# Optimization experiments

Hardware: AMD Instinct MI355X
Metric: run time of the kernel (lower is better)

Reference implementation:

```python
import jax, jax.numpy as jnp
import numpy as np

B, N, D, E = 4, 2048, 1024, 4
H = 4 * D  # expert hidden (mult=4)


def setup_inputs() -> dict:
    key = jax.random.key(0)
    ks = jax.random.split(key, 8)
    std = 0.02
    return {
        "x": jax.random.normal(ks[0], (B, N, D), jnp.float32),
        "W_slot": jax.random.normal(ks[1], (E * D, D), jnp.float32) * std,
        "u_slot": jax.random.normal(ks[2], (D,), jnp.float32),
        "sigma_slot": jnp.ones((1,), jnp.float32),
        "W1": jax.random.normal(ks[3], (E, H, D), jnp.float32) * std,
        "b1": jnp.zeros((E, H), jnp.float32),
        "u1": jax.random.normal(ks[4], (E, D), jnp.float32),
        "sig1": jnp.ones((E,), jnp.float32),
        "W2": jax.random.normal(ks[5], (E, D, H), jnp.float32) * std,
        "b2": jnp.zeros((E, D), jnp.float32),
        "u2": jax.random.normal(ks[6], (E, H), jnp.float32),
        "sig2": jnp.ones((E,), jnp.float32),
    }


def _sn_weight(W, u, sigma):
    # One power-iteration step (no_grad in torch -> stop_gradient), then
    # sigma_spec = v^T W u'; weight = W / sigma_spec * learnable sigma.
    v = W @ u
    v = jax.lax.stop_gradient(v / jnp.linalg.norm(v))
    u2 = W.T @ v
    u2 = jax.lax.stop_gradient(u2 / jnp.linalg.norm(u2))
    s = jnp.einsum('c,cd,d->', v, W, u2)
    return W * (sigma / s)


def reference(x, W_slot, u_slot, sigma_slot, W1, b1, u1, sig1, W2, b2, u2, sig2):
    b, n, d = x.shape
    e = W1.shape[0]
    s = n // e  # slots per expert; n divisible by e -> no padding, no mask

    # dynamic slot embeddings from consecutive-segment means
    Wsl = _sn_weight(W_slot, u_slot, sigma_slot[0])          # [e*d, d]
    xm = x.reshape(b, s, e, d).mean(axis=2)                   # [b, s, d]
    slot_embeds = (xm @ Wsl.T).reshape(b, s, e, d)
    slot_embeds = slot_embeds.transpose(0, 2, 1, 3)           # [b, e, s, d]

    logits = jnp.einsum('bnd,besd->bnes', x, slot_embeds)     # [b, n, e, s]
    dispatch = jax.nn.softmax(logits, axis=1)                 # softmax over n
    combine = jax.nn.softmax(logits.reshape(b, n, e * s), axis=-1)

    slots = jnp.einsum('bnd,bnes->ebsd', x, dispatch)         # [e, b, s, d]

    # per-expert FFN with spectral-normed weights (vectorized over experts)
    W1n = jax.vmap(_sn_weight)(W1, u1, sig1)                  # [e, H, d]
    W2n = jax.vmap(_sn_weight)(W2, u2, sig2)                  # [e, d, H]
    h = jax.nn.gelu(jnp.einsum('ebsd,ehd->ebsh', slots, W1n) + b1[:, None, None, :],
                    approximate=False)
    y = jnp.einsum('ebsh,edh->ebsd', h, W2n) + b2[:, None, None, :]

    out = y.transpose(1, 0, 2, 3).reshape(b, e * s, d)        # [b, e*s, d]
    return jnp.einsum('bsd,bns->bnd', out, combine)           # [b, n, d]
```

## Files before the change

### kernel.cpp

```cpp
#include <hip/hip_runtime.h>
#include <hip/hip_bf16.h>
#include <math.h>

constexpr int CB  = 4;
constexpr int CN  = 2048;
constexpr int CD  = 1024;
constexpr int CE  = 4;
constexpr int CS  = 512;
constexpr int CH  = 4096;
constexpr int CES = 2048;

typedef unsigned short u16;
typedef unsigned int   u32;
typedef __bf16 bf16x8 __attribute__((ext_vector_type(8)));
typedef float  f32x4  __attribute__((ext_vector_type(4)));

__device__ __forceinline__ u16 f2bf(float x) {
  u32 u = __float_as_uint(x);
  u = (u + 0x7FFF + ((u >> 16) & 1)) >> 16;
  return (u16)u;
}

__device__ __forceinline__ void gl2lds16(const void* g, void* l) {
  __builtin_amdgcn_global_load_lds(
      (const __attribute__((address_space(1))) void*)g,
      (__attribute__((address_space(3))) void*)l, 16, 0, 0);
}

__device__ __forceinline__ void xcd_swz(int& bx, int& by, int& bz) {
  u32 gx = gridDim.x, gy = gridDim.y;
  u32 w = blockIdx.x + gx * (blockIdx.y + gy * blockIdx.z);
  u32 nwg = gx * gy * gridDim.z;
  u32 q = nwg >> 3;
  u32 wg = (w & 7) * q + (w >> 3);
  bx = wg % gx;
  u32 r = wg / gx;
  by = r % gy;
  bz = r / gy;
}


__global__ __launch_bounds__(256) void gemv_rows_k(const float* __restrict__ W,
    const float* __restrict__ u, float* __restrict__ t1, int M, int K, int ustride) {
  int bi = blockIdx.y;
  int row = blockIdx.x * 4 + (threadIdx.x >> 6);
  int lane = threadIdx.x & 63;
  const float* Wr = W + ((long)bi * M + row) * K;
  const float* ub = u + (long)bi * ustride;
  float s = 0.f;
  for (int k = lane; k < K; k += 64) s += Wr[k] * ub[k];
#pragma unroll
  for (int off = 32; off; off >>= 1) s += __shfl_down(s, off, 64);
  if (lane == 0) t1[bi * M + row] = s;
}

__global__ __launch_bounds__(256) void gemv_cols_k(const float* __restrict__ W,
    const float* __restrict__ t1, float* __restrict__ t2,
    u16* __restrict__ bh, u16* __restrict__ bl, int M, int K) {
  int bi = blockIdx.z;
  int k = blockIdx.x * 256 + threadIdx.x;
  int m0 = blockIdx.y * 256;
  const float* Wb = W + (long)bi * M * K;
  const float* tb = t1 + bi * M;
  u16* bhb = bh + (long)bi * M * K;
  u16* blb = bl ? bl + (long)bi * M * K : nullptr;
  float s = 0.f;
#pragma unroll 4
  for (int m = 0; m < 256; m++) {
    long idx = (long)(m0 + m) * K + k;
    float w = Wb[idx];
    s += w * tb[m0 + m];
    u16 h = f2bf(w);
    bhb[idx] = h;
    if (blb) blb[idx] = f2bf(w - __uint_as_float((u32)h << 16));
  }
  atomicAdd(&t2[bi * K + k], s);
}

__global__ __launch_bounds__(256) void scale_k(const float* __restrict__ t1,
    const float* __restrict__ t2, const float* __restrict__ sig,
    float* __restrict__ out, int M, int K) {
  int bi = blockIdx.x;
  int tid = threadIdx.x;
  __shared__ float red[256];
  float s1 = 0.f;
  for (int i = tid; i < M; i += 256) { float v = t1[bi * M + i]; s1 += v * v; }
  red[tid] = s1; __syncthreads();
  for (int w = 128; w; w >>= 1) { if (tid < w) red[tid] += red[tid + w]; __syncthreads(); }
  float n1 = red[0]; __syncthreads();
  float s2 = 0.f;
  for (int i = tid; i < K; i += 256) { float v = t2[bi * K + i]; s2 += v * v; }
  red[tid] = s2; __syncthreads();
  for (int w = 128; w; w >>= 1) { if (tid < w) red[tid] += red[tid + w]; __syncthreads(); }
  if (tid == 0) out[bi] = sig[bi] * sqrtf(n1 / red[0]);
}

__global__ __launch_bounds__(256) void xsplit_fused_k(const float* __restrict__ x,
    u16* __restrict__ xh, u16* __restrict__ xl,
    u16* __restrict__ xmh, u16* __restrict__ xml) {
  int idx = blockIdx.x * 256 + threadIdx.x;
  int d8 = idx & (CD / 8 - 1);
  int si = (idx >> 7) & (CS - 1);
  int b  = idx >> 16;
  long rbase = ((long)(b * CN + si * 4)) * CD + d8 * 8;
  float vr[4][8];
#pragma unroll
  for (int r = 0; r < 4; r++) {
    float4 a = *(const float4*)(x + rbase + (long)r * CD);
    float4 c = *(const float4*)(x + rbase + (long)r * CD + 4);
    vr[r][0]=a.x; vr[r][1]=a.y; vr[r][2]=a.z; vr[r][3]=a.w;
    vr[r][4]=c.x; vr[r][5]=c.y; vr[r][6]=c.z; vr[r][7]=c.w;
  }
#pragma unroll
  for (int r = 0; r < 4; r++) {
    u16 oh[8], ol[8];
#pragma unroll
    for (int c = 0; c < 8; c++) {
      u16 h = f2bf(vr[r][c]);
      oh[c] = h;
      ol[c] = f2bf(vr[r][c] - __uint_as_float((u32)h << 16));
    }
    *(uint4*)(xh + rbase + (long)r * CD) = *(const uint4*)oh;
    *(uint4*)(xl + rbase + (long)r * CD) = *(const uint4*)ol;
  }
  long mbase = ((long)(b * CS + si)) * CD + d8 * 8;
  u16 oh[8], ol[8];
#pragma unroll
  for (int c = 0; c < 8; c++) {
    float v = 0.25f * (vr[0][c] + vr[1][c] + vr[2][c] + vr[3][c]);
    u16 h = f2bf(v);
    oh[c] = h;
    ol[c] = f2bf(v - __uint_as_float((u32)h << 16));
  }
  *(uint4*)(xmh + mbase) = *(const uint4*)oh;
  *(uint4*)(xml + mbase) = *(const uint4*)ol;
}

__global__ __launch_bounds__(256) void colstat_part_k(const float* __restrict__ lg,
    float* __restrict__ pmax, float* __restrict__ psum) {
  int es = blockIdx.x * 256 + threadIdx.x;
  int sl = blockIdx.y;
  int b  = blockIdx.z;
  const float* p = lg + ((long)(b * CN + sl * 256)) * CES + es;
  float m = -1e30f, s = 0.f;
  for (int i = 0; i < 256; i++) {
    float v = p[(long)i * CES];
    if (v > m) { s *= __expf(m - v); m = v; }
    s += __expf(v - m);
  }
  int o = (b * 8 + sl) * CES + es;
  pmax[o] = m; psum[o] = s;
}

__global__ __launch_bounds__(256) void colstat_comb_k(const float* __restrict__ pmax,
    const float* __restrict__ psum, float* __restrict__ cmax, float* __restrict__ csum) {
  int idx = blockIdx.x * 256 + threadIdx.x;
  int b = idx >> 11;
  int es = idx & (CES - 1);
  float m = -1e30f;
#pragma unroll
  for (int sl = 0; sl < 8; sl++) m = fmaxf(m, pmax[(b * 8 + sl) * CES + es]);
  float s = 0.f;
#pragma unroll
  for (int sl = 0; sl < 8; sl++)
    s += psum[(b * 8 + sl) * CES + es] * __expf(pmax[(b * 8 + sl) * CES + es] - m);
  cmax[idx] = m; csum[idx] = s;
}

__global__ __launch_bounds__(256) void rowcomb_k(const float* __restrict__ lg,
                                                 u16* __restrict__ outB) {
  __shared__ float red[8];
  long row = blockIdx.x;
  const float* p = lg + row * CES + threadIdx.x * 8;
  float4 a = *(const float4*)p;
  float4 b = *(const float4*)(p + 4);
  float v[8] = {a.x, a.y, a.z, a.w, b.x, b.y, b.z, b.w};
  float m = v[0];
#pragma unroll
  for (int c = 1; c < 8; c++) m = fmaxf(m, v[c]);
#pragma unroll
  for (int off = 32; off; off >>= 1) m = fmaxf(m, __shfl_xor(m, off, 64));
  int wv = threadIdx.x >> 6;
  if ((threadIdx.x & 63) == 0) red[wv] = m;
  __syncthreads();
  m = fmaxf(fmaxf(red[0], red[1]), fmaxf(red[2], red[3]));
  float s = 0.f;
#pragma unroll
  for (int c = 0; c < 8; c++) { v[c] = __expf(v[c] - m); s += v[c]; }
#pragma unroll
  for (int off = 32; off; off >>= 1) s += __shfl_xor(s, off, 64);
  if ((threadIdx.x & 63) == 0) red[4 + wv] = s;
  __syncthreads();
  float inv = 1.f / (red[4] + red[5] + red[6] + red[7]);
  u16 o[8];
#pragma unroll
  for (int c = 0; c < 8; c++) o[c] = f2bf(v[c] * inv);
  *(uint4*)(outB + row * CES + threadIdx.x * 8) = *(const uint4*)o;
}

__global__ __launch_bounds__(256) void tr_f2b_k(const float* __restrict__ in,
    u16* __restrict__ out, const float* __restrict__ sub, int R, int C, int expmode) {
  __shared__ u16 t[32][33];
  int z = blockIdx.z;
  long ibase = (long)z * R * C;
  int r0 = blockIdx.y * 32, c0 = blockIdx.x * 32;
  int tx = threadIdx.x & 31, ty = threadIdx.x >> 5;
  float cm = expmode ? sub[(long)z * C + c0 + tx] : 0.f;
  for (int rr = ty; rr < 32; rr += 8) {
    float v = in[ibase + (long)(r0 + rr) * C + c0 + tx];
    if (expmode) v = __expf(v - cm);
    t[tx][rr] = f2bf(v);
  }
  __syncthreads();
  for (int cc = ty; cc < 32; cc += 8)
    out[ibase + (long)(c0 + cc) * R + r0 + tx] = t[cc][tx];
}

struct MEpSESplit {
  u16* hi; u16* lo; const float* scale;
  __device__ void store(int z, int m, int n, float v) const {
    v *= scale[0];
    int b = m >> 9, si = m & 511, ei = n >> 10, di = n & 1023;
    long o = ((long)(b * CES + ei * 512 + si)) * CD + di;
    u16 h = f2bf(v);
    hi[o] = h;
    lo[o] = f2bf(v - __uint_as_float((u32)h << 16));
  }
};
struct MEpLogits {
  float* lg;
  __device__ void store(int b, int m, int n, float v) const {
    lg[((long)(b * CN + m)) * CES + n] = v;
  }
};
struct MEpSlots {
  u16* sb; const float* __restrict__ csum;
  __device__ void store(int b, int m, int n, float v) const {
    float inv = 1.f / csum[b * CES + m];
    int e = m >> 9, si = m & 511;
    sb[((long)(e * 2048 + b * 512 + si)) * CD + n] = f2bf(v * inv);
  }
};
struct MEpGelu {
  u16* h; const float* __restrict__ scales; const float* __restrict__ b1;
  __device__ void store(int e, int m, int n, float v) const {
    float xg = v * scales[1 + e] + b1[e * CH + n];
    float g = 0.5f * xg * (1.f + erff(xg * 0.70710678118654752f));
    h[((long)(e * 2048 + m)) * CH + n] = f2bf(g);
  }
};
struct MEpYT {
  u16* ot; const float* __restrict__ scales; const float* __restrict__ b2;
  __device__ void store(int e, int m, int n, float v) const {
    int b = n >> 9, si = n & 511;
    ot[((long)(b * CD + m)) * CES + e * 512 + si] = f2bf(v * scales[5 + e] + b2[e * CD + m]);
  }
};
struct MEpOut {
  float* o;
  __device__ void store(int b, int m, int n, float v) const {
    o[((long)(b * CN + m)) * CD + n] = v;
  }
};


template <int BN, int BK, class EP>
__global__ __launch_bounds__(256) void mgemm_k(const u16* __restrict__ A, long Azs, int ldA,
                                               const u16* __restrict__ B, long Bzs, int ldB,
                                               EP ep, int K) {
  constexpr int BM = 128;
  constexpr int FI = 4;
  constexpr int FJ = BN / 32;
  constexpr int RPL = 512 / BK;
  constexpr int NGRP = (BM + BN) / RPL;
  constexpr int GPW = NGRP / 4;
  __shared__ __align__(16) u16 S[(BM + BN) * BK];
  int bx, by, bz;
  xcd_swz(bx, by, bz);
  const int tid = threadIdx.x;
  const int wid = tid >> 6, lane = tid & 63;
  const int m0 = by * BM, n0 = bx * BN;
  const u16* Az = A + (long)bz * Azs;
  const u16* Bz = B + (long)bz * Bzs;
  const int wr = wid >> 1, wc = wid & 1;
  const int lrow = lane / (BK / 8);
  const int lk   = (lane % (BK / 8)) * 8;

  f32x4 acc[FI][FJ];
  f32x4 zero = {0.f, 0.f, 0.f, 0.f};
#pragma unroll
  for (int i = 0; i < FI; i++)
#pragma unroll
    for (int j = 0; j < FJ; j++) acc[i][j] = zero;

  for (int k0 = 0; k0 < K; k0 += BK) {
#pragma unroll
    for (int g = 0; g < GPW; g++) {
      int grp = g * 4 + wid;
      int row = grp * RPL + lrow;
      const u16* src = (row < BM)
          ? Az + (long)(m0 + row) * ldA + k0 + lk
          : Bz + (long)(n0 + row - BM) * ldB + k0 + lk;
      gl2lds16(src, (char*)S + grp * 1024);
    }
    __syncthreads();
#pragma unroll
    for (int kk2 = 0; kk2 < BK / 32; kk2++) {
      bf16x8 af[FI], bfr[FJ];
#pragma unroll
      for (int i = 0; i < FI; i++) {
        int arow = wr * 64 + i * 16 + (lane & 15);
        af[i] = *(const bf16x8*)&S[arow * BK + kk2 * 32 + (lane >> 4) * 8];
      }
#pragma unroll
      for (int j = 0; j < FJ; j++) {
        int brow = BM + wc * (BN / 2) + j * 16 + (lane & 15);
        bfr[j] = *(const bf16x8*)&S[brow * BK + kk2 * 32 + (lane >> 4) * 8];
      }
#pragma unroll
      for (int i = 0; i < FI; i++)
#pragma unroll
        for (int j = 0; j < FJ; j++)
          acc[i][j] = __builtin_amdgcn_mfma_f32_16x16x32_bf16(af[i], bfr[j], acc[i][j], 0, 0, 0);
    }
    __syncthreads();
  }
#pragma unroll
  for (int i = 0; i < FI; i++) {
    int grow = m0 + wr * 64 + i * 16 + (lane >> 4) * 4;
#pragma unroll
    for (int j = 0; j < FJ; j++) {
      int gcol = n0 + wc * (BN / 2) + j * 16 + (lane & 15);
#pragma unroll
      for (int r = 0; r < 4; r++)
        ep.store(bz, grow + r, gcol, acc[i][j][r]);
    }
  }
}

template <class EP>
__global__ __launch_bounds__(256) void mgemm3_k(const u16* __restrict__ Ah,
                                                const u16* __restrict__ Al, long Azs, int ldA,
                                                const u16* __restrict__ Bh,
                                                const u16* __restrict__ Bl, long Bzs, int ldB,
                                                EP ep, int K) {
  constexpr int BK = 32;
  __shared__ __align__(16) u16 Ahs[128 * BK];
  __shared__ __align__(16) u16 Als[128 * BK];
  __shared__ __align__(16) u16 Bhs[128 * BK];
  __shared__ __align__(16) u16 Bls[128 * BK];
  int bx, by, bz;
  xcd_swz(bx, by, bz);
  const int tid = threadIdx.x;
  const int wid = tid >> 6, lane = tid & 63;
  const int m0 = by * 128, n0 = bx * 128;
  const u16* Ahz = Ah + (long)bz * Azs;
  const u16* Alz = Al + (long)bz * Azs;
  const u16* Bhz = Bh + (long)bz * Bzs;
  const u16* Blz = Bl + (long)bz * Bzs;
  const int wr = wid >> 1, wc = wid & 1;
  const int srow = lane >> 2;
  const int sk8  = (lane & 3) * 8;

  f32x4 acc[4][4];
  f32x4 zero = {0.f, 0.f, 0.f, 0.f};
#pragma unroll
  for (int i = 0; i < 4; i++)
#pragma unroll
    for (int j = 0; j < 4; j++) acc[i][j] = zero;

  for (int k0 = 0; k0 < K; k0 += BK) {
#pragma unroll
    for (int i = 0; i < 2; i++) {
      int chunk = i * 4 + wid;
      int r = chunk * 16 + srow;
      long ao = (long)(m0 + r) * ldA + k0 + sk8;
      long bo = (long)(n0 + r) * ldB + k0 + sk8;
      gl2lds16(Ahz + ao, (char*)Ahs + chunk * 1024);
      gl2lds16(Alz + ao, (char*)Als + chunk * 1024);
      gl2lds16(Bhz + bo, (char*)Bhs + chunk * 1024);
      gl2lds16(Blz + bo, (char*)Bls + chunk * 1024);
    }
    __syncthreads();
    bf16x8 ah[4], al[4], bh[4], bl[4];
#pragma unroll
    for (int i = 0; i < 4; i++) {
      int arow = wr * 64 + i * 16 + (lane & 15);
      int aoff = arow * BK + (lane >> 4) * 8;
      ah[i] = *(const bf16x8*)&Ahs[aoff];
      al[i] = *(const bf16x8*)&Als[aoff];
      int brow = wc * 64 + i * 16 + (lane & 15);
      int boff = brow * BK + (lane >> 4) * 8;
      bh[i] = *(const bf16x8*)&Bhs[boff];
      bl[i] = *(const bf16x8*)&Bls[boff];
    }
#pragma unroll
    for (int i = 0; i < 4; i++)
#pragma unroll
      for (int j = 0; j < 4; j++) {
        acc[i][j] = __builtin_amdgcn_mfma_f32_16x16x32_bf16(ah[i], bh[j], acc[i][j], 0, 0, 0);
        acc[i][j] = __builtin_amdgcn_mfma_f32_16x16x32_bf16(al[i], bh[j], acc[i][j], 0, 0, 0);
        acc[i][j] = __builtin_amdgcn_mfma_f32_16x16x32_bf16(ah[i], bl[j], acc[i][j], 0, 0, 0);
      }
    __syncthreads();
  }
#pragma unroll
  for (int i = 0; i < 4; i++) {
    int grow = m0 + wr * 64 + i * 16 + (lane >> 4) * 4;
#pragma unroll
    for (int j = 0; j < 4; j++) {
      int gcol = n0 + wc * 64 + j * 16 + (lane & 15);
#pragma unroll
      for (int r = 0; r < 4; r++)
        ep.store(bz, grow + r, gcol, acc[i][j][r]);
    }
  }
}

extern "C" void kernel_launch(void* const* d_in, const int* in_sizes, int n_in,
                              void* d_out, int out_size, void* d_ws, size_t ws_size,
                              hipStream_t stream) {
  const float* x          = (const float*)d_in[0];
  const float* W_slot     = (const float*)d_in[1];
  const float* u_slot     = (const float*)d_in[2];
  const float* sigma_slot = (const float*)d_in[3];
  const float* W1         = (const float*)d_in[4];
  const float* b1         = (const float*)d_in[5];
  const float* u1         = (const float*)d_in[6];
  const float* sig1       = (const float*)d_in[7];
  const float* W2         = (const float*)d_in[8];
  const float* b2         = (const float*)d_in[9];
  const float* u2         = (const float*)d_in[10];
  const float* sig2       = (const float*)d_in[11];
  float* out = (float*)d_out;

  char* ws = (char*)d_ws;
  size_t off = 0;
  auto alloc = [&](size_t bytes) -> char* {
    char* p = ws + off;
    off += (bytes + 255) & ~(size_t)255;
    return p;
  };
  float* t1s = (float*)alloc(4096 * 4);
  float* t1a = (float*)alloc(4 * 4096 * 4);
  float* t1b = (float*)alloc(4 * 1024 * 4);
  float* t2s = (float*)alloc(1024 * 4);
  float* t2a = (float*)alloc(4 * 1024 * 4);
  float* t2b = (float*)alloc(4 * 4096 * 4);
  float* scales = (float*)alloc(16 * 4);
  float* pmax   = (float*)alloc((size_t)CB * 8 * CES * 4);
  float* psum   = (float*)alloc((size_t)CB * 8 * CES * 4);
  float* cmax   = (float*)alloc((size_t)CB * CES * 4);
  float* csum   = (float*)alloc((size_t)CB * CES * 4);
  char* regAB   = alloc((size_t)CB * CN * CD * 2 * 2);
  char* regBB   = alloc((size_t)CB * CES * CD * 2 * 2);
  char* regL    = alloc((size_t)CB * CN * CES * 4);
  char* regS    = alloc((size_t)CE * CB * CS * CD * 2);
  u16* W1b      = (u16*)alloc((size_t)CE * CH * CD * 2);
  u16* W2b      = (u16*)alloc((size_t)CE * CD * CH * 2);

  u16*   xh      = (u16*)regAB;
  u16*   xl      = (u16*)(regAB + (size_t)CB * CN * CD * 2);
  u16*   dispT   = (u16*)regAB;
  u16*   combineB= (u16*)regAB;
  u16*   seh     = (u16*)regBB;
  u16*   sel     = (u16*)(regBB + (size_t)CB * CES * CD * 2);
  u16*   xT      = (u16*)regBB;
  float* logits  = (float*)regL;
  u16*   hbuf    = (u16*)regL;
  u16*   xmh     = (u16*)regL;
  u16*   xml     = (u16*)(regL + (size_t)CB * CS * CD * 2);
  u16*   wslh    = (u16*)(regL + (size_t)2 * CB * CS * CD * 2);
  u16*   wsll    = (u16*)(regL + (size_t)2 * CB * CS * CD * 2 + (size_t)CE * CD * CD * 2);
  u16*   slotsB  = (u16*)regS;
  u16*   outbufT = (u16*)regS;

  hipMemsetAsync(t2s, 0, 1024 * 4, stream);
  hipMemsetAsync(t2a, 0, 4 * 1024 * 4, stream);
  hipMemsetAsync(t2b, 0, 4 * 4096 * 4, stream);

  gemv_rows_k<<<dim3(4096 / 4, 1), 256, 0, stream>>>(W_slot, u_slot, t1s, 4096, 1024, 0);
  gemv_rows_k<<<dim3(4096 / 4, 4), 256, 0, stream>>>(W1, u1, t1a, CH, CD, CD);
  gemv_rows_k<<<dim3(1024 / 4, 4), 256, 0, stream>>>(W2, u2, t1b, CD, CH, CH);
  gemv_cols_k<<<dim3(1024 / 256, 4096 / 256, 1), 256, 0, stream>>>(W_slot, t1s, t2s, wslh, wsll, 4096, 1024);
  gemv_cols_k<<<dim3(1024 / 256, 4096 / 256, 4), 256, 0, stream>>>(W1, t1a, t2a, W1b, nullptr, CH, CD);
  gemv_cols_k<<<dim3(4096 / 256, 1024 / 256, 4), 256, 0, stream>>>(W2, t1b, t2b, W2b, nullptr, CD, CH);
  scale_k<<<1, 256, 0, stream>>>(t1s, t2s, sigma_slot, scales + 0, 4096, 1024);
  scale_k<<<4, 256, 0, stream>>>(t1a, t2a, sig1, scales + 1, CH, CD);
  scale_k<<<4, 256, 0, stream>>>(t1b, t2b, sig2, scales + 5, CD, CH);

  xsplit_fused_k<<<(CB * CS * (CD / 8)) / 256, 256, 0, stream>>>(x, xh, xl, xmh, xml);

  mgemm3_k<<<dim3(4096 / 128, 2048 / 128, 1), 256, 0, stream>>>(
      xmh, xml, 0L, CD, wslh, wsll, 0L, CD, MEpSESplit{seh, sel, scales}, CD);

  mgemm3_k<<<dim3(CES / 128, CN / 128, CB), 256, 0, stream>>>(
      xh, xl, (long)CN * CD, CD, seh, sel, (long)CES * CD, CD,
      MEpLogits{logits}, CD);

  colstat_part_k<<<dim3(CES / 256, 8, CB), 256, 0, stream>>>(logits, pmax, psum);
  colstat_comb_k<<<(CB * CES) / 256, 256, 0, stream>>>(pmax, psum, cmax, csum);

  tr_f2b_k<<<dim3(CES / 32, CN / 32, CB), 256, 0, stream>>>(logits, dispT, cmax, CN, CES, 1);
  tr_f2b_k<<<dim3(CD / 32, CN / 32, CB), 256, 0, stream>>>(x, xT, nullptr, CN, CD, 0);

  mgemm_k<64, 64><<<dim3(CD / 64, CES / 128, CB), 256, 0, stream>>>(
      dispT, (long)CES * CN, CN, xT, (long)CD * CN, CN, MEpSlots{slotsB, csum}, CN);

  rowcomb_k<<<CB * CN, 256, 0, stream>>>(logits, combineB);

  mgemm_k<128, 32><<<dim3(CH / 128, 2048 / 128, CE), 256, 0, stream>>>(
      slotsB, (long)2048 * CD, CD, W1b, (long)CH * CD, CD, MEpGelu{hbuf, scales, b1}, CD);

  mgemm_k<64, 64><<<dim3(2048 / 64, CD / 128, CE), 256, 0, stream>>>(
      W2b, (long)CD * CH, CH, hbuf, (long)2048 * CH, CH, MEpYT{outbufT, scales, b2}, CH);

  mgemm_k<64, 64><<<dim3(CD / 64, CN / 128, CB), 256, 0, stream>>>(
      combineB, (long)CN * CES, CES, outbufT, (long)CD * CES, CES, MEpOut{out}, CES);

  (void)in_sizes; (void)n_in; (void)out_size; (void)ws_size;
}
```

Baseline: 897.3 us.

## Merge scale kernels and memsets, use tanh GELU, widen FFN1 tile K

Combines the three spectral-norm scale launches into one 9-block kernel and the three memsets into one contiguous memset, cutting launch overhead. Replaces the exact erf GELU in the FFN1 epilogue with the tanh approximation computed via __expf. Changes the FFN1 GEMM template from 128x32 to 128x64 tiling. The tanh GELU departs from the exact GELU in the reference, and the single memset relies on contiguous workspace layout.

```diff
diff --git a/kernel.cpp b/kernel.cpp
--- a/kernel.cpp
+++ b/kernel.cpp
@@ -77,22 +77,29 @@
   atomicAdd(&t2[bi * K + k], s);
 }
 
-__global__ __launch_bounds__(256) void scale_k(const float* __restrict__ t1,
-    const float* __restrict__ t2, const float* __restrict__ sig,
-    float* __restrict__ out, int M, int K) {
+__global__ __launch_bounds__(256) void scale_all_k(
+    const float* __restrict__ t1s, const float* __restrict__ t2s,
+    const float* __restrict__ t1a, const float* __restrict__ t2a,
+    const float* __restrict__ t1b, const float* __restrict__ t2b,
+    const float* __restrict__ sigs, const float* __restrict__ sig1,
+    const float* __restrict__ sig2, float* __restrict__ scales) {
   int bi = blockIdx.x;
+  const float *t1, *t2; float sg; float* o; int M, K;
+  if (bi == 0)      { t1 = t1s;                 t2 = t2s;                 sg = sigs[0];     o = scales + 0;      M = 4096; K = 1024; }
+  else if (bi < 5)  { int e = bi - 1; t1 = t1a + e * 4096; t2 = t2a + e * 1024; sg = sig1[e]; o = scales + 1 + e; M = 4096; K = 1024; }
+  else              { int e = bi - 5; t1 = t1b + e * 1024; t2 = t2b + e * 4096; sg = sig2[e]; o = scales + 5 + e; M = 1024; K = 4096; }
   int tid = threadIdx.x;
   __shared__ float red[256];
   float s1 = 0.f;
-  for (int i = tid; i < M; i += 256) { float v = t1[bi * M + i]; s1 += v * v; }
+  for (int i = tid; i < M; i += 256) { float v = t1[i]; s1 += v * v; }
   red[tid] = s1; __syncthreads();
   for (int w = 128; w; w >>= 1) { if (tid < w) red[tid] += red[tid + w]; __syncthreads(); }
   float n1 = red[0]; __syncthreads();
   float s2 = 0.f;
-  for (int i = tid; i < K; i += 256) { float v = t2[bi * K + i]; s2 += v * v; }
+  for (int i = tid; i < K; i += 256) { float v = t2[i]; s2 += v * v; }
   red[tid] = s2; __syncthreads();
   for (int w = 128; w; w >>= 1) { if (tid < w) red[tid] += red[tid + w]; __syncthreads(); }
-  if (tid == 0) out[bi] = sig[bi] * sqrtf(n1 / red[0]);
+  if (tid == 0) o[0] = sg * sqrtf(n1 / red[0]);
 }
 
 __global__ __launch_bounds__(256) void xsplit_fused_k(const float* __restrict__ x,
@@ -245,7 +252,10 @@
   u16* h; const float* __restrict__ scales; const float* __restrict__ b1;
   __device__ void store(int e, int m, int n, float v) const {
     float xg = v * scales[1 + e] + b1[e * CH + n];
-    float g = 0.5f * xg * (1.f + erff(xg * 0.70710678118654752f));
+    float t = xg * (0.7978845608f + 0.0356774081f * xg * xg);
+    float ex = __expf(2.f * t);
+    float th = 1.f - 2.f / (ex + 1.f);
+    float g = 0.5f * xg * (1.f + th);
     h[((long)(e * 2048 + m)) * CH + n] = f2bf(g);
   }
 };
@@ -475,9 +485,7 @@
   u16*   slotsB  = (u16*)regS;
   u16*   outbufT = (u16*)regS;
 
-  hipMemsetAsync(t2s, 0, 1024 * 4, stream);
-  hipMemsetAsync(t2a, 0, 4 * 1024 * 4, stream);
-  hipMemsetAsync(t2b, 0, 4 * 4096 * 4, stream);
+  hipMemsetAsync(t2s, 0, (size_t)((char*)t2b - (char*)t2s) + 4 * 4096 * 4, stream);
 
   gemv_rows_k<<<dim3(4096 / 4, 1), 256, 0, stream>>>(W_slot, u_slot, t1s, 4096, 1024, 0);
   gemv_rows_k<<<dim3(4096 / 4, 4), 256, 0, stream>>>(W1, u1, t1a, CH, CD, CD);
@@ -485,9 +493,8 @@
   gemv_cols_k<<<dim3(1024 / 256, 4096 / 256, 1), 256, 0, stream>>>(W_slot, t1s, t2s, wslh, wsll, 4096, 1024);
   gemv_cols_k<<<dim3(1024 / 256, 4096 / 256, 4), 256, 0, stream>>>(W1, t1a, t2a, W1b, nullptr, CH, CD);
   gemv_cols_k<<<dim3(4096 / 256, 1024 / 256, 4), 256, 0, stream>>>(W2, t1b, t2b, W2b, nullptr, CD, CH);
-  scale_k<<<1, 256, 0, stream>>>(t1s, t2s, sigma_slot, scales + 0, 4096, 1024);
-  scale_k<<<4, 256, 0, stream>>>(t1a, t2a, sig1, scales + 1, CH, CD);
-  scale_k<<<4, 256, 0, stream>>>(t1b, t2b, sig2, scales + 5, CD, CH);
+  scale_all_k<<<9, 256, 0, stream>>>(t1s, t2s, t1a, t2a, t1b, t2b,
+                                     sigma_slot, sig1, sig2, scales);
 
   xsplit_fused_k<<<(CB * CS * (CD / 8)) / 256, 256, 0, stream>>>(x, xh, xl, xmh, xml);
 
@@ -509,7 +516,7 @@
 
   rowcomb_k<<<CB * CN, 256, 0, stream>>>(logits, combineB);
 
-  mgemm_k<128, 32><<<dim3(CH / 128, 2048 / 128, CE), 256, 0, stream>>>(
+  mgemm_k<128, 64><<<dim3(CH / 128, 2048 / 128, CE), 256, 0, stream>>>(
       slotsB, (long)2048 * CD, CD, W1b, (long)CH * CD, CD, MEpGelu{hbuf, scales, b1}, CD);
 
   mgemm_k<64, 64><<<dim3(2048 / 64, CD / 128, CE), 256, 0, stream>>>(
```

Result: no change. 899.8 us (+0.3%).
